# Optimization experiments

Hardware: AMD Instinct MI355X
Metric: run time of the kernel (lower is better)

The kernel has to match this reference:

```python
import jax, jax.numpy as jnp
import numpy as np

B, T, D, E, V, EXTRA = 32, 1024, 512, 256, 50257, 200


def setup_inputs() -> dict:
    key = jax.random.key(0)
    ks = jax.random.split(key, 20)
    s = 0.02
    rn = lambda k, shape: jax.random.normal(k, shape, dtype=jnp.float32) * s
    inp = {}
    inp["decoder_input"] = jax.random.randint(ks[0], (B,), 0, V)
    inp["h0"] = rn(ks[1], (B, D))
    inp["c0"] = rn(ks[2], (B, D))
    inp["encoder_outputs"] = rn(ks[3], (B, T, 2 * D))
    inp["encoder_pad_mask"] = jnp.ones((B, T), jnp.float32)
    inp["previous_context_vector"] = rn(ks[4], (B, 2 * D))
    inp["coverage"] = jax.random.uniform(ks[5], (B, T), jnp.float32) * 0.01
    inp["extra_zeros"] = jnp.zeros((B, EXTRA), jnp.float32)
    inp["encoder_input_extra_vocabs"] = jax.random.randint(ks[6], (B, T), 0, V + EXTRA)
    inp["step"] = 1
    inp["embedding"] = rn(ks[7], (V, E))
    inp["W_gx"] = rn(ks[8], (2 * D + E, E)); inp["b_gx"] = jnp.zeros((E,), jnp.float32)
    inp["W_ih"] = rn(ks[9], (E, 4 * D)); inp["W_hh"] = rn(ks[10], (D, 4 * D))
    inp["b_ih"] = jnp.zeros((4 * D,), jnp.float32); inp["b_hh"] = jnp.zeros((4 * D,), jnp.float32)
    inp["W_h"] = rn(ks[11], (2 * D, 2 * D))
    inp["W_c"] = rn(ks[12], (2 * D,))
    inp["W_s"] = rn(ks[13], (2 * D, 2 * D)); inp["b_s"] = jnp.zeros((2 * D,), jnp.float32)
    inp["v"] = rn(ks[14], (2 * D,))
    inp["W_pg"] = rn(ks[15], (4 * D + E,)); inp["b_pg"] = jnp.zeros((1,), jnp.float32)
    inp["W_v1"] = rn(ks[16], (3 * D, D)); inp["b_v1"] = jnp.zeros((D,), jnp.float32)
    inp["W_v2"] = rn(ks[17], (D, V)); inp["b_v2"] = jnp.zeros((V,), jnp.float32)
    return inp


def reference(decoder_input, h0, c0, encoder_outputs, encoder_pad_mask,
              previous_context_vector, coverage, extra_zeros,
              encoder_input_extra_vocabs, step,
              embedding, W_gx, b_gx, W_ih, W_hh, b_ih, b_hh,
              W_h, W_c, W_s, b_s, v, W_pg, b_pg, W_v1, b_v1, W_v2, b_v2):
    # Pointer-generator decoder single step (training path / step>0), coverage on.
    softmax_temperature = 1.0
    emb = embedding[decoder_input]                                  # [B,E]
    x = jnp.concatenate([previous_context_vector, emb], -1) @ W_gx + b_gx  # [B,E]
    # LSTM cell, torch gate order (i, f, g, o)
    gates = x @ W_ih + h0 @ W_hh + b_ih + b_hh                      # [B,4D]
    i, f, g, o = jnp.split(gates, 4, axis=-1)
    c1 = jax.nn.sigmoid(f) * c0 + jax.nn.sigmoid(i) * jnp.tanh(g)
    h1 = jax.nn.sigmoid(o) * jnp.tanh(c1)                           # [B,D]
    dec_hat = jnp.concatenate([h1, c1], -1)                         # [B,2D]
    # Bahdanau additive attention with coverage feature
    enc_feat = encoder_outputs @ W_h                                # [B,T,2D]
    dec_feat = dec_hat @ W_s + b_s                                  # [B,2D]
    cov_feat = coverage[..., None] * W_c                            # [B,T,2D]
    energy = jnp.tanh(enc_feat + dec_feat[:, None, :] + cov_feat)
    scores = energy @ v                                             # [B,T]
    att = jax.nn.softmax(scores / softmax_temperature, axis=-1) * encoder_pad_mask
    att = att / att.sum(-1, keepdims=True)                          # renormalized
    context = jnp.einsum('bt,btd->bd', att, encoder_outputs)        # [B,2D]
    coverage_next = coverage + att
    # pointer-generator gate
    pg_in = jnp.concatenate([context, dec_hat, x], -1)              # [B,4D+E]
    p_gen = jax.nn.sigmoid(pg_in @ W_pg + b_pg)[:, None]            # [B,1]
    out = jnp.concatenate([h1, context], -1)                        # [B,3D]
    logits = ((out @ W_v1 + b_v1) @ W_v2 + b_v2) / softmax_temperature
    vocab_dist = jax.nn.softmax(logits, axis=-1)                    # [B,V]
    vd_oov = jnp.concatenate([p_gen * vocab_dist, extra_zeros], 1)  # [B,V+EXTRA]
    att_oov = (1.0 - p_gen) * att                                   # [B,T]
    rows = jnp.arange(B)[:, None]
    vocab_dist_final = vd_oov.at[rows, encoder_input_extra_vocabs].add(att_oov)
    return (vocab_dist_final, (h1, c1), context, att, coverage_next)
```

## Files before the change

### kernel.cpp

```cpp
#include <hip/hip_runtime.h>
#include <hip/hip_bf16.h>

typedef __attribute__((ext_vector_type(4))) float f32x4;
typedef __attribute__((ext_vector_type(8))) short s16x8;
typedef __attribute__((ext_vector_type(4))) short s16x4;

#define DEVINL __device__ __forceinline__

static constexpr int BB = 32, TT = 1024, DD = 512, EE = 256, VV = 50257, EXTRA = 200;
static constexpr int D2 = 1024;
static constexpr int VE = VV + EXTRA;
static constexpr long MM = (long)BB * TT;
static constexpr int VPAD = 50304;
static constexpr int NBLK = 786;

DEVINL unsigned short f2bf(float x) {
    union { float f; unsigned int u; } c; c.f = x;
    unsigned int u = c.u;
    u += 0x7fffu + ((u >> 16) & 1u);
    return (unsigned short)(u >> 16);
}
DEVINL float bf2f(unsigned short h) {
    union { unsigned int u; float f; } c; c.u = ((unsigned int)h) << 16;
    return c.f;
}
DEVINL float sigmoidf_(float x) { return 1.0f / (1.0f + __expf(-x)); }
DEVINL float tanh_fast(float x) {
    x = fminf(15.f, fmaxf(-15.f, x));
    float e = __expf(2.f * x);
    return (e - 1.f) / (e + 1.f);
}
DEVINL void gl16(const void* g, void* l) {
    __builtin_amdgcn_global_load_lds((__attribute__((address_space(1))) void*)g,
                                     (__attribute__((address_space(3))) void*)l, 16, 0, 0);
}

__global__ __launch_bounds__(256) void k_prep(const float* __restrict__ Wh,
                                              const float* __restrict__ enc,
                                              unsigned short* __restrict__ WhT,
                                              unsigned short* __restrict__ encswz) {
    __shared__ float tile[32][33];
    const int bid = blockIdx.x, tid = threadIdx.x;
    if (bid < 1024) {
        int n0 = (bid & 31) * 32, k0 = (bid >> 5) * 32;
        int col = tid & 31, row = tid >> 5;
        #pragma unroll
        for (int i = 0; i < 4; i++)
            tile[row + i * 8][col] = Wh[(long)(k0 + row + i * 8) * D2 + n0 + col];
        __syncthreads();
        #pragma unroll
        for (int i = 0; i < 4; i++) {
            int n = n0 + row + i * 8;
            int kcol = (k0 + col) ^ ((n & 7) << 3);
            WhT[(long)n * D2 + kcol] = f2bf(tile[col][row + i * 8]);
        }
    } else {
        long idx = (long)(bid - 1024) * 256 + tid;
        int m  = (int)(idx >> 7);
        int k2 = (int)(idx & 127) * 8;
        int s  = (m & 7) << 3;
        const float* src = enc + (long)m * 1024 + (k2 ^ s);
        f32x4 a = *(const f32x4*)src;
        f32x4 b = *(const f32x4*)(src + 4);
        s16x8 h;
        h[0] = (short)f2bf(a[0]); h[1] = (short)f2bf(a[1]); h[2] = (short)f2bf(a[2]); h[3] = (short)f2bf(a[3]);
        h[4] = (short)f2bf(b[0]); h[5] = (short)f2bf(b[1]); h[6] = (short)f2bf(b[2]); h[7] = (short)f2bf(b[3]);
        *(s16x8*)(encswz + (long)m * 1024 + k2) = h;
    }
}

__global__ __launch_bounds__(512) void k_x(
    const int* __restrict__ dec_in, const float* __restrict__ pcv,
    const float* __restrict__ embt, const float* __restrict__ Wgx,
    const float* __restrict__ bgx, float* __restrict__ xbuf) {
    __shared__ float xs[1280];
    __shared__ float sred[8][64];
    int b = blockIdx.x, n0 = blockIdx.y * 64;
    int tid = threadIdx.x, nl = tid & 63, ks = tid >> 6;
    long er = (long)dec_in[b] * EE;
    for (int i = tid; i < 1280; i += 512)
        xs[i] = (i < 1024) ? pcv[b * 1024 + i] : embt[er + i - 1024];
    __syncthreads();
    float acc = 0.f;
    for (int k = ks * 160; k < ks * 160 + 160; ++k)
        acc += xs[k] * Wgx[(long)k * EE + n0 + nl];
    sred[ks][nl] = acc;
    __syncthreads();
    if (tid < 64) {
        int n = n0 + tid;
        float s = bgx[n];
        #pragma unroll
        for (int i = 0; i < 8; i++) s += sred[i][tid];
        xbuf[b * EE + n] = s;
    }
}

__global__ __launch_bounds__(512) void k_lstm(
    const float* __restrict__ xbuf, const float* __restrict__ h0,
    const float* __restrict__ c0, const float* __restrict__ Wih,
    const float* __restrict__ Whh, const float* __restrict__ bih,
    const float* __restrict__ bhh, float* __restrict__ h1o,
    float* __restrict__ c1o, float* __restrict__ dechat) {
    __shared__ float xs[768];
    __shared__ float sred[4][8][64];
    int b = blockIdx.x, d0 = blockIdx.y * 64;
    int tid = threadIdx.x, dl = tid & 63, ks = tid >> 6;
    for (int i = tid; i < 768; i += 512)
        xs[i] = (i < 256) ? xbuf[b * 256 + i] : h0[b * 512 + i - 256];
    __syncthreads();
    float a0 = 0, a1 = 0, a2 = 0, a3 = 0;
    for (int k = ks * 96; k < ks * 96 + 96; ++k) {
        float xv = xs[k];
        const float* wr = (k < 256) ? (Wih + (long)k * 2048) : (Whh + (long)(k - 256) * 2048);
        a0 += xv * wr[d0 + dl];        a1 += xv * wr[512 + d0 + dl];
        a2 += xv * wr[1024 + d0 + dl]; a3 += xv * wr[1536 + d0 + dl];
    }
    sred[0][ks][dl] = a0; sred[1][ks][dl] = a1; sred[2][ks][dl] = a2; sred[3][ks][dl] = a3;
    __syncthreads();
    if (tid < 64) {
        int d = d0 + tid;
        float gi = bih[d] + bhh[d];
        float gf = bih[512 + d] + bhh[512 + d];
        float gg = bih[1024 + d] + bhh[1024 + d];
        float go = bih[1536 + d] + bhh[1536 + d];
        #pragma unroll
        for (int s = 0; s < 8; s++) {
            gi += sred[0][s][tid]; gf += sred[1][s][tid];
            gg += sred[2][s][tid]; go += sred[3][s][tid];
        }
        float c1 = sigmoidf_(gf) * c0[b * 512 + d] + sigmoidf_(gi) * tanh_fast(gg);
        float h1 = sigmoidf_(go) * tanh_fast(c1);
        h1o[b * 512 + d] = h1; c1o[b * 512 + d] = c1;
        dechat[b * 1024 + d] = h1; dechat[b * 1024 + 512 + d] = c1;
    }
}

__global__ __launch_bounds__(512) void k_decfeat(
    const float* __restrict__ dechat, const float* __restrict__ Ws,
    const float* __restrict__ bs, float* __restrict__ decfeat) {
    __shared__ float xs[1024];
    __shared__ float sred[8][64];
    int b = blockIdx.x, n0 = blockIdx.y * 64;
    int tid = threadIdx.x, nl = tid & 63, ks = tid >> 6;
    for (int i = tid; i < 1024; i += 512) xs[i] = dechat[b * 1024 + i];
    __syncthreads();
    float acc = 0.f;
    for (int k = ks * 128; k < ks * 128 + 128; ++k)
        acc += xs[k] * Ws[(long)k * 1024 + n0 + nl];
    sred[ks][nl] = acc;
    __syncthreads();
    if (tid < 64) {
        int n = n0 + tid;
        float s = bs[n];
        #pragma unroll
        for (int i = 0; i < 8; i++) s += sred[i][tid];
        decfeat[b * 1024 + n] = s;
    }
}

__global__ __launch_bounds__(512) void k_scores(
    const unsigned short* __restrict__ encswz, const unsigned short* __restrict__ whtswz,
    const float* __restrict__ decfeat, const float* __restrict__ cov,
    const float* __restrict__ Wc, const float* __restrict__ vvec,
    float* __restrict__ scorep) {
    __shared__ __align__(16) unsigned short As[128 * 64];
    __shared__ __align__(16) unsigned short Bs[256 * 64];
    __shared__ float sred[4][128];
    const int tid = threadIdx.x;
    const int lane = tid & 63, wave = tid >> 6;
    const int wid = __builtin_amdgcn_readfirstlane(wave);
    const int g = lane >> 4, c = lane & 15;
    const int wm = wave >> 2, wn = wave & 3;

    const int bid = blockIdx.x;
    const int xcd = bid & 7, t = bid >> 3;
    const int mt = xcd * 32 + (t >> 2), nt = t & 3;
    const long m0 = (long)mt * 128;
    const int n0 = nt * 256;
    const int bblk = mt >> 3;

    const int arow = wid * 16 + (lane >> 3);
    const int axo  = (lane & 7) * 8;
    const int brow = wid * 32 + (lane >> 3);
    unsigned short* aBase = &As[wid * 1024];
    unsigned short* bBase = &Bs[wid * 2048];

    f32x4 acc[4][4];
    #pragma unroll
    for (int i = 0; i < 4; i++)
        #pragma unroll
        for (int j = 0; j < 4; j++) acc[i][j] = (f32x4){0.f, 0.f, 0.f, 0.f};

    const int sx = (c & 7) << 3;

    for (int kt = 0; kt < 16; ++kt) {
        const int k0 = kt * 64;
        __syncthreads();
        gl16(encswz + (m0 + arow) * 1024 + k0 + axo,       aBase);
        gl16(encswz + (m0 + arow + 8) * 1024 + k0 + axo,   aBase + 512);
        gl16(whtswz + (long)(n0 + brow) * 1024 + k0 + axo,        bBase);
        gl16(whtswz + (long)(n0 + brow + 8) * 1024 + k0 + axo,    bBase + 512);
        gl16(whtswz + (long)(n0 + brow + 16) * 1024 + k0 + axo,   bBase + 1024);
        gl16(whtswz + (long)(n0 + brow + 24) * 1024 + k0 + axo,   bBase + 1536);
        __syncthreads();
        #pragma unroll
        for (int kk = 0; kk < 2; ++kk) {
            const int kse = (kk * 32 + g * 8) ^ sx;
            s16x8 af[4], bfj[4];
            #pragma unroll
            for (int i = 0; i < 4; i++) af[i] = *(const s16x8*)&As[(wm * 64 + i * 16 + c) * 64 + kse];
            #pragma unroll
            for (int j = 0; j < 4; j++) bfj[j] = *(const s16x8*)&Bs[(wn * 64 + j * 16 + c) * 64 + kse];
            #pragma unroll
            for (int i = 0; i < 4; i++)
                #pragma unroll
                for (int j = 0; j < 4; j++)
                    acc[i][j] = __builtin_amdgcn_mfma_f32_16x16x32_bf16(af[i], bfj[j], acc[i][j], 0, 0, 0);
        }
    }
    float dfv[4], wcv[4], vvj[4];
    #pragma unroll
    for (int j = 0; j < 4; j++) {
        int col = n0 + wn * 64 + j * 16 + c;
        dfv[j] = decfeat[bblk * D2 + col];
        wcv[j] = Wc[col];
        vvj[j] = vvec[col];
    }
    float sAcc[4][4];
    #pragma unroll
    for (int i = 0; i < 4; i++) {
        #pragma unroll
        for (int r = 0; r < 4; r++) {
            const long m = m0 + wm * 64 + i * 16 + g * 4 + r;
            const float covm = cov[m];
            float su = 0.f;
            #pragma unroll
            for (int j = 0; j < 4; j++) {
                float e = acc[i][j][r] + dfv[j] + covm * wcv[j];
                su += tanh_fast(e) * vvj[j];
            }
            su += __shfl_xor(su, 1); su += __shfl_xor(su, 2);
            su += __shfl_xor(su, 4); su += __shfl_xor(su, 8);
            sAcc[i][r] = su;
        }
    }
    if (c == 0) {
        #pragma unroll
        for (int i = 0; i < 4; i++)
            #pragma unroll
            for (int r = 0; r < 4; r++)
                sred[wn][wm * 64 + i * 16 + g * 4 + r] = sAcc[i][r];
    }
    __syncthreads();
    if (tid < 128)
        scorep[(long)nt * MM + m0 + tid] = sred[0][tid] + sred[1][tid] + sred[2][tid] + sred[3][tid];
}

__global__ void k_softmax(const float* __restrict__ scorep, const float* __restrict__ mask,
                          const float* __restrict__ cov, float* __restrict__ att,
                          float* __restrict__ covn) {
    int b = blockIdx.x, tid = threadIdx.x;
    __shared__ float sm[8];
    float sv[4];
    float mx = -1e30f;
    #pragma unroll
    for (int i = 0; i < 4; i++) {
        long idx = (long)b * TT + tid + 256 * i;
        sv[i] = scorep[idx] + scorep[MM + idx] + scorep[2 * MM + idx] + scorep[3 * MM + idx];
        mx = fmaxf(mx, sv[i]);
    }
    for (int o = 32; o; o >>= 1) mx = fmaxf(mx, __shfl_xor(mx, o));
    if ((tid & 63) == 0) sm[tid >> 6] = mx;
    __syncthreads();
    mx = fmaxf(fmaxf(sm[0], sm[1]), fmaxf(sm[2], sm[3]));
    __syncthreads();
    float e[4]; float s = 0.f;
    #pragma unroll
    for (int i = 0; i < 4; i++) { e[i] = __expf(sv[i] - mx); s += e[i]; }
    for (int o = 32; o; o >>= 1) s += __shfl_xor(s, o);
    if ((tid & 63) == 0) sm[tid >> 6] = s;
    __syncthreads();
    s = sm[0] + sm[1] + sm[2] + sm[3];
    __syncthreads();
    float inv = 1.f / s;
    float am[4]; float s2 = 0.f;
    #pragma unroll
    for (int i = 0; i < 4; i++) { am[i] = e[i] * inv * mask[b * TT + tid + 256 * i]; s2 += am[i]; }
    for (int o = 32; o; o >>= 1) s2 += __shfl_xor(s2, o);
    if ((tid & 63) == 0) sm[tid >> 6] = s2;
    __syncthreads();
    s2 = sm[0] + sm[1] + sm[2] + sm[3];
    float inv2 = 1.f / s2;
    #pragma unroll
    for (int i = 0; i < 4; i++) {
        int t = tid + 256 * i;
        float a = am[i] * inv2;
        att[b * TT + t] = a;
        covn[b * TT + t] = cov[b * TT + t] + a;
    }
}

__global__ void k_context(const unsigned short* __restrict__ encswz, const float* __restrict__ att,
                          float* __restrict__ part) {
    int b = blockIdx.x, tc = blockIdx.y;
    int d4 = threadIdx.x;
    float a0 = 0, a1 = 0, a2 = 0, a3 = 0;
    const float* ab = att + b * TT;
    for (int t = tc * 64; t < tc * 64 + 64; ++t) {
        float a = ab[t];
        int sx = (t & 7) << 3;
        const unsigned short* ep = encswz + ((long)b * TT + t) * D2 + ((d4 * 4) ^ sx);
        s16x4 ev = *(const s16x4*)ep;
        a0 += a * bf2f((unsigned short)ev[0]); a1 += a * bf2f((unsigned short)ev[1]);
        a2 += a * bf2f((unsigned short)ev[2]); a3 += a * bf2f((unsigned short)ev[3]);
    }
    float* pp = part + (long)tc * BB * D2 + b * D2 + d4 * 4;
    pp[0] = a0; pp[1] = a1; pp[2] = a2; pp[3] = a3;
}

__global__ __launch_bounds__(1024) void k_ctxpgen(
    const float* __restrict__ part, const float* __restrict__ dechat,
    const float* __restrict__ xbuf, const float* __restrict__ Wpg,
    const float* __restrict__ bpg, float* __restrict__ ctx,
    float* __restrict__ pgen) {
    int b = blockIdx.x, tid = threadIdx.x;
    __shared__ float sm[16];
    float s = 0.f;
    #pragma unroll
    for (int p = 0; p < 16; p++) s += part[(long)p * BB * D2 + b * D2 + tid];
    ctx[b * D2 + tid] = s;
    float pacc = s * Wpg[tid] + dechat[b * D2 + tid] * Wpg[D2 + tid];
    if (tid < EE) pacc += xbuf[b * EE + tid] * Wpg[2 * D2 + tid];
    for (int o = 32; o; o >>= 1) pacc += __shfl_xor(pacc, o);
    if ((tid & 63) == 0) sm[tid >> 6] = pacc;
    __syncthreads();
    if (tid == 0) {
        float t = 0.f;
        #pragma unroll
        for (int i = 0; i < 16; i++) t += sm[i];
        pgen[b] = sigmoidf_(t + bpg[0]);
    }
}

__global__ __launch_bounds__(512) void k_hidden(
    const float* __restrict__ h1, const float* __restrict__ ctx,
    const float* __restrict__ Wv1, const float* __restrict__ bv1,
    unsigned short* __restrict__ hbf) {
    __shared__ float xs[1536];
    __shared__ float sred[8][64];
    int b = blockIdx.x, n0 = blockIdx.y * 64;
    int tid = threadIdx.x, nl = tid & 63, ks = tid >> 6;
    for (int i = tid; i < 1536; i += 512)
        xs[i] = (i < 512) ? h1[b * 512 + i] : ctx[b * 1024 + i - 512];
    __syncthreads();
    float acc = 0.f;
    for (int k = ks * 192; k < ks * 192 + 192; ++k)
        acc += xs[k] * Wv1[(long)k * 512 + n0 + nl];
    sred[ks][nl] = acc;
    __syncthreads();
    if (tid < 64) {
        int n = n0 + tid;
        float s = bv1[n];
        #pragma unroll
        for (int i = 0; i < 8; i++) s += sred[i][tid];
        hbf[b * 512 + n] = f2bf(s);
    }
}

__global__ __launch_bounds__(256) void k_logits(const unsigned short* __restrict__ hbf,
                                                const float* __restrict__ Wv2,
                                                const float* __restrict__ bv2,
                                                float* __restrict__ logits,
                                                float* __restrict__ bsm,
                                                float* __restrict__ bss) {
    constexpr int PITCH = 136;
    __shared__ __align__(16) unsigned short Bs[64 * PITCH];
    __shared__ float sm_[4][16], ss_[4][16];
    const int tid = threadIdx.x;
    const int lane = tid & 63, wave = tid >> 6;
    const int g = lane >> 4, c = lane & 15;
    const int wm = wave >> 1, wn = wave & 1;
    const long v0 = (long)blockIdx.x * 64;
    const bool tail = (v0 + 64 > VV);

    const int vg = tid & 15, kr = tid >> 4;

    f32x4 acc[2];
    acc[0] = (f32x4){0.f, 0.f, 0.f, 0.f};
    acc[1] = (f32x4){0.f, 0.f, 0.f, 0.f};
    const int sxr = (c & 7) << 3;

    for (int kt = 0; kt < 4; ++kt) {
        const int k0 = kt * 128;
        __syncthreads();
        #pragma unroll
        for (int pi = 0; pi < 4; ++pi) {
            const int ka = k0 + kr * 8 + pi * 2;
            f32x4 wa, wb;
            if (!tail) {
                wa = *(const f32x4*)&Wv2[(long)ka * VV + v0 + vg * 4];
                wb = *(const f32x4*)&Wv2[(long)(ka + 1) * VV + v0 + vg * 4];
            } else {
                #pragma unroll
                for (int j = 0; j < 4; j++) {
                    long v = v0 + vg * 4 + j;
                    long vs = (v < VV) ? v : (VV - 1);
                    wa[j] = Wv2[(long)ka * VV + vs];
                    wb[j] = Wv2[(long)(ka + 1) * VV + vs];
                }
            }
            #pragma unroll
            for (int j = 0; j < 4; j++) {
                int vl = vg * 4 + j;
                int ks = (kr * 8 + pi * 2) ^ ((vl & 7) << 3);
                unsigned int pack = (unsigned int)f2bf(wa[j]) | ((unsigned int)f2bf(wb[j]) << 16);
                *(unsigned int*)&Bs[vl * PITCH + ks] = pack;
            }
        }
        __syncthreads();
        #pragma unroll
        for (int kk = 0; kk < 4; ++kk) {
            const int koff = kk * 32 + g * 8;
            const int kse = koff ^ sxr;
            s16x8 af = *(const s16x8*)&hbf[(wm * 16 + c) * 512 + k0 + koff];
            s16x8 bf0 = *(const s16x8*)&Bs[(wn * 32 + c) * PITCH + kse];
            s16x8 bf1 = *(const s16x8*)&Bs[(wn * 32 + 16 + c) * PITCH + kse];
            acc[0] = __builtin_amdgcn_mfma_f32_16x16x32_bf16(af, bf0, acc[0], 0, 0, 0);
            acc[1] = __builtin_amdgcn_mfma_f32_16x16x32_bf16(af, bf1, acc[1], 0, 0, 0);
        }
    }
    float lv[2][4];
    #pragma unroll
    for (int j = 0; j < 2; j++) {
        long v = v0 + wn * 32 + j * 16 + c;
        bool valid = (v < VV);
        float bvv = valid ? bv2[v] : 0.f;
        #pragma unroll
        for (int r = 0; r < 4; r++) {
            float val = acc[j][r] + bvv;
            if (valid) {
                int b = wm * 16 + g * 4 + r;
                logits[(long)b * VV + v] = val;
                lv[j][r] = val;
            } else {
                lv[j][r] = -1e30f;
            }
        }
    }
    float mrow[4], srow[4];
    #pragma unroll
    for (int r = 0; r < 4; r++) {
        float m = fmaxf(lv[0][r], lv[1][r]);
        m = fmaxf(m, __shfl_xor(m, 1)); m = fmaxf(m, __shfl_xor(m, 2));
        m = fmaxf(m, __shfl_xor(m, 4)); m = fmaxf(m, __shfl_xor(m, 8));
        float s = __expf(lv[0][r] - m) + __expf(lv[1][r] - m);
        s += __shfl_xor(s, 1); s += __shfl_xor(s, 2);
        s += __shfl_xor(s, 4); s += __shfl_xor(s, 8);
        mrow[r] = m; srow[r] = s;
    }
    if (c == 0) {
        #pragma unroll
        for (int r = 0; r < 4; r++) { sm_[wave][g * 4 + r] = mrow[r]; ss_[wave][g * 4 + r] = srow[r]; }
    }
    __syncthreads();
    if (tid < 32) {
        int b = tid;
        int w0 = (b >> 4) * 2, ridx = b & 15;
        float mA = sm_[w0][ridx], mB = sm_[w0 + 1][ridx];
        float sA = ss_[w0][ridx], sB = ss_[w0 + 1][ridx];
        float m = fmaxf(mA, mB);
        float s = sA * __expf(mA - m) + sB * __expf(mB - m);
        bsm[(long)b * NBLK + blockIdx.x] = m;
        bss[(long)b * NBLK + blockIdx.x] = s;
    }
}

__global__ __launch_bounds__(1024) void k_vocab_all(
    const float* __restrict__ logits, const float* __restrict__ bsm,
    const float* __restrict__ bss, const float* __restrict__ pgen,
    const float* __restrict__ extraz, const float* __restrict__ att,
    const int* __restrict__ eiv, float* __restrict__ out0) {
    int b = blockIdx.x, tid = threadIdx.x;
    __shared__ float sm[16];
    float mi = -1e30f, si = 0.f;
    if (tid < NBLK) { mi = bsm[(long)b * NBLK + tid]; si = bss[(long)b * NBLK + tid]; }
    float mx = mi;
    for (int o = 32; o; o >>= 1) mx = fmaxf(mx, __shfl_xor(mx, o));
    if ((tid & 63) == 0) sm[tid >> 6] = mx;
    __syncthreads();
    mx = sm[0];
    #pragma unroll
    for (int i = 1; i < 16; i++) mx = fmaxf(mx, sm[i]);
    __syncthreads();
    float s = si * __expf(mi - mx);
    for (int o = 32; o; o >>= 1) s += __shfl_xor(s, o);
    if ((tid & 63) == 0) sm[tid >> 6] = s;
    __syncthreads();
    s = 0.f;
    #pragma unroll
    for (int i = 0; i < 16; i++) s += sm[i];
    float pg = pgen[b];
    float inv = pg / s;
    const float* lr = logits + (long)b * VV;
    float* orow = out0 + (long)b * VE;
    for (int v = tid; v < VV; v += 1024) orow[v] = __expf(lr[v] - mx) * inv;
    if (tid < EXTRA) orow[VV + tid] = extraz[b * EXTRA + tid];
    __syncthreads();
    float a = (1.f - pg) * att[b * TT + tid];
    atomicAdd(orow + eiv[b * TT + tid], a);
}

extern "C" void kernel_launch(void* const* d_in, const int* in_sizes, int n_in,
                              void* d_out, int out_size, void* d_ws, size_t ws_size,
                              hipStream_t stream) {
    const int*   dec_in = (const int*)d_in[0];
    const float* h0     = (const float*)d_in[1];
    const float* c0     = (const float*)d_in[2];
    const float* enc    = (const float*)d_in[3];
    const float* mask   = (const float*)d_in[4];
    const float* pcv    = (const float*)d_in[5];
    const float* cov    = (const float*)d_in[6];
    const float* extraz = (const float*)d_in[7];
    const int*   eiv    = (const int*)d_in[8];
    const float* embt   = (const float*)d_in[10];
    const float* Wgx    = (const float*)d_in[11];
    const float* bgx    = (const float*)d_in[12];
    const float* Wih    = (const float*)d_in[13];
    const float* Whh    = (const float*)d_in[14];
    const float* bih    = (const float*)d_in[15];
    const float* bhh    = (const float*)d_in[16];
    const float* Wh     = (const float*)d_in[17];
    const float* Wc     = (const float*)d_in[18];
    const float* Ws     = (const float*)d_in[19];
    const float* bs     = (const float*)d_in[20];
    const float* vv     = (const float*)d_in[21];
    const float* Wpg    = (const float*)d_in[22];
    const float* bpg    = (const float*)d_in[23];
    const float* Wv1    = (const float*)d_in[24];
    const float* bv1    = (const float*)d_in[25];
    const float* Wv2    = (const float*)d_in[26];
    const float* bv2    = (const float*)d_in[27];

    float* out = (float*)d_out;
    float* out_vd  = out;
    float* out_h1  = out + (long)BB * VE;
    float* out_c1  = out_h1 + BB * DD;
    float* out_ctx = out_c1 + BB * DD;
    float* out_att = out_ctx + BB * D2;
    float* out_cov = out_att + BB * TT;

    char* p = (char*)d_ws;
    unsigned short* whtswz = (unsigned short*)p; p += (size_t)D2 * D2 * 2;
    float* xbuf    = (float*)p;  p += (size_t)BB * EE * 4;
    float* dechat  = (float*)p;  p += (size_t)BB * D2 * 4;
    float* decfeat = (float*)p;  p += (size_t)BB * D2 * 4;
    float* scorep  = (float*)p;  p += (size_t)4 * MM * 4;
    float* pgen    = (float*)p;  p += 256;
    unsigned short* hbf = (unsigned short*)p; p += (size_t)BB * DD * 2 + 256;
    float* bsm     = (float*)p;  p += (size_t)BB * NBLK * 4;
    float* bss     = (float*)p;  p += (size_t)BB * NBLK * 4;
    float* ctxpart = (float*)p;  p += (size_t)16 * BB * D2 * 4;
    float* logits  = (float*)p;  p += (size_t)BB * VV * 4;
    unsigned short* encswz = (unsigned short*)p; p += (size_t)MM * D2 * 2;

    k_prep<<<1024 + 16384, 256, 0, stream>>>(Wh, enc, whtswz, encswz);
    k_x<<<dim3(BB, 4), 512, 0, stream>>>(dec_in, pcv, embt, Wgx, bgx, xbuf);
    k_lstm<<<dim3(BB, 8), 512, 0, stream>>>(xbuf, h0, c0, Wih, Whh, bih, bhh, out_h1, out_c1, dechat);
    k_decfeat<<<dim3(BB, 16), 512, 0, stream>>>(dechat, Ws, bs, decfeat);
    k_scores<<<1024, 512, 0, stream>>>(encswz, whtswz, decfeat, cov, Wc, vv, scorep);
    k_softmax<<<BB, 256, 0, stream>>>(scorep, mask, cov, out_att, out_cov);
    k_context<<<dim3(BB, 16), 256, 0, stream>>>(encswz, out_att, ctxpart);
    k_ctxpgen<<<BB, 1024, 0, stream>>>(ctxpart, dechat, xbuf, Wpg, bpg, out_ctx, pgen);
    k_hidden<<<dim3(BB, 8), 512, 0, stream>>>(out_h1, out_ctx, Wv1, bv1, hbf);
    k_logits<<<NBLK, 256, 0, stream>>>(hbf, Wv2, bv2, logits, bsm, bss);
    k_vocab_all<<<BB, 1024, 0, stream>>>(logits, bsm, bss, pgen, extraz, out_att, eiv, out_vd);
}
```

Before: 241.4 us.

## Split vocab finalize into parallel kernels, widen context loads, prefetch Wv2 tiles

The final vocab kernel, which ran only 32 blocks, is split into three kernels: a per-row stats reduction, a vocab write spread over a 32x25 grid, and an atomic scatter. The point is to use more of the GPU for the large output write. The context kernel now reads 8 bf16 values per thread and splits time steps across two thread halves, producing 32 partial sums instead of 16. The logits GEMM loads the next k-tile of Wv2 into registers while the current one is stored to shared memory. The cost is two extra kernel launches, more register pressure in the logits kernel, and a larger partial-sum buffer to reduce.

```diff
diff --git a/kernel.cpp b/kernel.cpp
--- a/kernel.cpp
+++ b/kernel.cpp
@@ -11,7 +11,6 @@
 static constexpr int D2 = 1024;
 static constexpr int VE = VV + EXTRA;
 static constexpr long MM = (long)BB * TT;
-static constexpr int VPAD = 50304;
 static constexpr int NBLK = 786;
 
 DEVINL unsigned short f2bf(float x) {
@@ -303,19 +302,24 @@
 __global__ void k_context(const unsigned short* __restrict__ encswz, const float* __restrict__ att,
                           float* __restrict__ part) {
     int b = blockIdx.x, tc = blockIdx.y;
-    int d4 = threadIdx.x;
-    float a0 = 0, a1 = 0, a2 = 0, a3 = 0;
+    int tid = threadIdx.x;
+    int d8 = (tid & 127) * 8;
+    int tofs = tid >> 7;
+    float a0 = 0, a1 = 0, a2 = 0, a3 = 0, a4 = 0, a5 = 0, a6 = 0, a7 = 0;
     const float* ab = att + b * TT;
-    for (int t = tc * 64; t < tc * 64 + 64; ++t) {
+    for (int t = tc * 64 + tofs; t < tc * 64 + 64; t += 2) {
         float a = ab[t];
         int sx = (t & 7) << 3;
-        const unsigned short* ep = encswz + ((long)b * TT + t) * D2 + ((d4 * 4) ^ sx);
-        s16x4 ev = *(const s16x4*)ep;
+        const unsigned short* ep = encswz + ((long)b * TT + t) * D2 + (d8 ^ sx);
+        s16x8 ev = *(const s16x8*)ep;
         a0 += a * bf2f((unsigned short)ev[0]); a1 += a * bf2f((unsigned short)ev[1]);
         a2 += a * bf2f((unsigned short)ev[2]); a3 += a * bf2f((unsigned short)ev[3]);
-    }
-    float* pp = part + (long)tc * BB * D2 + b * D2 + d4 * 4;
+        a4 += a * bf2f((unsigned short)ev[4]); a5 += a * bf2f((unsigned short)ev[5]);
+        a6 += a * bf2f((unsigned short)ev[6]); a7 += a * bf2f((unsigned short)ev[7]);
+    }
+    float* pp = part + (long)(tc * 2 + tofs) * BB * D2 + b * D2 + d8;
     pp[0] = a0; pp[1] = a1; pp[2] = a2; pp[3] = a3;
+    pp[4] = a4; pp[5] = a5; pp[6] = a6; pp[7] = a7;
 }
 
 __global__ __launch_bounds__(1024) void k_ctxpgen(
@@ -327,7 +331,7 @@
     __shared__ float sm[16];
     float s = 0.f;
     #pragma unroll
-    for (int p = 0; p < 16; p++) s += part[(long)p * BB * D2 + b * D2 + tid];
+    for (int p = 0; p < 32; p++) s += part[(long)p * BB * D2 + b * D2 + tid];
     ctx[b * D2 + tid] = s;
     float pacc = s * Wpg[tid] + dechat[b * D2 + tid] * Wpg[D2 + tid];
     if (tid < EE) pacc += xbuf[b * EE + tid] * Wpg[2 * D2 + tid];
@@ -390,31 +394,54 @@
     acc[1] = (f32x4){0.f, 0.f, 0.f, 0.f};
     const int sxr = (c & 7) << 3;
 
+    f32x4 wa[4], wb[4];
+    #pragma unroll
+    for (int pi = 0; pi < 4; ++pi) {
+        const int ka = kr * 8 + pi * 2;
+        if (!tail) {
+            wa[pi] = *(const f32x4*)&Wv2[(long)ka * VV + v0 + vg * 4];
+            wb[pi] = *(const f32x4*)&Wv2[(long)(ka + 1) * VV + v0 + vg * 4];
+        } else {
+            #pragma unroll
+            for (int j = 0; j < 4; j++) {
+                long v = v0 + vg * 4 + j;
+                long vs = (v < VV) ? v : (VV - 1);
+                wa[pi][j] = Wv2[(long)ka * VV + vs];
+                wb[pi][j] = Wv2[(long)(ka + 1) * VV + vs];
+            }
+        }
+    }
+    #pragma unroll
     for (int kt = 0; kt < 4; ++kt) {
         const int k0 = kt * 128;
         __syncthreads();
         #pragma unroll
         for (int pi = 0; pi < 4; ++pi) {
-            const int ka = k0 + kr * 8 + pi * 2;
-            f32x4 wa, wb;
-            if (!tail) {
-                wa = *(const f32x4*)&Wv2[(long)ka * VV + v0 + vg * 4];
-                wb = *(const f32x4*)&Wv2[(long)(ka + 1) * VV + v0 + vg * 4];
-            } else {
-                #pragma unroll
-                for (int j = 0; j < 4; j++) {
-                    long v = v0 + vg * 4 + j;
-                    long vs = (v < VV) ? v : (VV - 1);
-                    wa[j] = Wv2[(long)ka * VV + vs];
-                    wb[j] = Wv2[(long)(ka + 1) * VV + vs];
-                }
-            }
             #pragma unroll
             for (int j = 0; j < 4; j++) {
                 int vl = vg * 4 + j;
                 int ks = (kr * 8 + pi * 2) ^ ((vl & 7) << 3);
-                unsigned int pack = (unsigned int)f2bf(wa[j]) | ((unsigned int)f2bf(wb[j]) << 16);
+                unsigned int pack = (unsigned int)f2bf(wa[pi][j]) | ((unsigned int)f2bf(wb[pi][j]) << 16);
                 *(unsigned int*)&Bs[vl * PITCH + ks] = pack;
+            }
+        }
+        if (kt < 3) {
+            const int k1 = (kt + 1) * 128;
+            #pragma unroll
+            for (int pi = 0; pi < 4; ++pi) {
+                const int ka = k1 + kr * 8 + pi * 2;
+                if (!tail) {
+                    wa[pi] = *(const f32x4*)&Wv2[(long)ka * VV + v0 + vg * 4];
+                    wb[pi] = *(const f32x4*)&Wv2[(long)(ka + 1) * VV + v0 + vg * 4];
+                } else {
+                    #pragma unroll
+                    for (int j = 0; j < 4; j++) {
+                        long v = v0 + vg * 4 + j;
+                        long vs = (v < VV) ? v : (VV - 1);
+                        wa[pi][j] = Wv2[(long)ka * VV + vs];
+                        wb[pi][j] = Wv2[(long)(ka + 1) * VV + vs];
+                    }
+                }
             }
         }
         __syncthreads();
@@ -475,15 +502,13 @@
     }
 }
 
-__global__ __launch_bounds__(1024) void k_vocab_all(
-    const float* __restrict__ logits, const float* __restrict__ bsm,
-    const float* __restrict__ bss, const float* __restrict__ pgen,
-    const float* __restrict__ extraz, const float* __restrict__ att,
-    const int* __restrict__ eiv, float* __restrict__ out0) {
+__global__ __launch_bounds__(1024) void k_finstats(
+    const float* __restrict__ bsm, const float* __restrict__ bss,
+    const float* __restrict__ pgen, float* __restrict__ stats2) {
     int b = blockIdx.x, tid = threadIdx.x;
     __shared__ float sm[16];
-    float mi = -1e30f, si = 0.f;
-    if (tid < NBLK) { mi = bsm[(long)b * NBLK + tid]; si = bss[(long)b * NBLK + tid]; }
+    float mi = (tid < NBLK) ? bsm[(long)b * NBLK + tid] : -1e30f;
+    float si = (tid < NBLK) ? bss[(long)b * NBLK + tid] : 0.f;
     float mx = mi;
     for (int o = 32; o; o >>= 1) mx = fmaxf(mx, __shfl_xor(mx, o));
     if ((tid & 63) == 0) sm[tid >> 6] = mx;
@@ -496,18 +521,38 @@
     for (int o = 32; o; o >>= 1) s += __shfl_xor(s, o);
     if ((tid & 63) == 0) sm[tid >> 6] = s;
     __syncthreads();
-    s = 0.f;
-    #pragma unroll
-    for (int i = 0; i < 16; i++) s += sm[i];
-    float pg = pgen[b];
-    float inv = pg / s;
+    if (tid == 0) {
+        s = 0.f;
+        #pragma unroll
+        for (int i = 0; i < 16; i++) s += sm[i];
+        stats2[b * 2]     = mx;
+        stats2[b * 2 + 1] = pgen[b] / s;
+    }
+}
+
+__global__ __launch_bounds__(512) void k_vocab_write(
+    const float* __restrict__ logits, const float* __restrict__ stats2,
+    const float* __restrict__ extraz, float* __restrict__ out0) {
+    int b = blockIdx.x;
+    int v0 = blockIdx.y * 2048;
+    int tid = threadIdx.x;
+    float mx = stats2[b * 2], inv = stats2[b * 2 + 1];
     const float* lr = logits + (long)b * VV;
     float* orow = out0 + (long)b * VE;
-    for (int v = tid; v < VV; v += 1024) orow[v] = __expf(lr[v] - mx) * inv;
-    if (tid < EXTRA) orow[VV + tid] = extraz[b * EXTRA + tid];
-    __syncthreads();
-    float a = (1.f - pg) * att[b * TT + tid];
-    atomicAdd(orow + eiv[b * TT + tid], a);
+    #pragma unroll
+    for (int i = 0; i < 4; i++) {
+        int v = v0 + i * 512 + tid;
+        if (v < VV)      orow[v] = __expf(lr[v] - mx) * inv;
+        else if (v < VE) orow[v] = extraz[b * EXTRA + (v - VV)];
+    }
+}
+
+__global__ __launch_bounds__(1024) void k_scatter(
+    const int* __restrict__ eiv, const float* __restrict__ att,
+    const float* __restrict__ pgen, float* __restrict__ out0) {
+    int b = blockIdx.x, tid = threadIdx.x;
+    float a = (1.f - pgen[b]) * att[b * TT + tid];
+    atomicAdd(out0 + (long)b * VE + eiv[b * TT + tid], a);
 }
 
 extern "C" void kernel_launch(void* const* d_in, const int* in_sizes, int n_in,
@@ -559,7 +604,8 @@
     unsigned short* hbf = (unsigned short*)p; p += (size_t)BB * DD * 2 + 256;
     float* bsm     = (float*)p;  p += (size_t)BB * NBLK * 4;
     float* bss     = (float*)p;  p += (size_t)BB * NBLK * 4;
-    float* ctxpart = (float*)p;  p += (size_t)16 * BB * D2 * 4;
+    float* stats2  = (float*)p;  p += 256;
+    float* ctxpart = (float*)p;  p += (size_t)32 * BB * D2 * 4;
     float* logits  = (float*)p;  p += (size_t)BB * VV * 4;
     unsigned short* encswz = (unsigned short*)p; p += (size_t)MM * D2 * 2;
 
@@ -573,5 +619,7 @@
     k_ctxpgen<<<BB, 1024, 0, stream>>>(ctxpart, dechat, xbuf, Wpg, bpg, out_ctx, pgen);
     k_hidden<<<dim3(BB, 8), 512, 0, stream>>>(out_h1, out_ctx, Wv1, bv1, hbf);
     k_logits<<<NBLK, 256, 0, stream>>>(hbf, Wv2, bv2, logits, bsm, bss);
-    k_vocab_all<<<BB, 1024, 0, stream>>>(logits, bsm, bss, pgen, extraz, out_att, eiv, out_vd);
-}
+    k_finstats<<<BB, 1024, 0, stream>>>(bsm, bss, pgen, stats2);
+    k_vocab_write<<<dim3(BB, 25), 512, 0, stream>>>(logits, stats2, extraz, out_vd);
+    k_scatter<<<BB, 1024, 0, stream>>>(eiv, out_att, pgen, out_vd);
+}
```

Result: no change. 239.9 us (-0.6%).
